# Kernel tuning notes

Measured on AMD Instinct MI355X. Metric: run time of the kernel, lower is better.

Reference implementation:

```python
import jax, jax.numpy as jnp
import numpy as np
from jax import lax

NUM_ENT = 100000
NUM_REL = 500
ENT_DIM = 100   # emb_dim1 * emb_dim2 = 10 * 10
REL_DIM = 2500  # 100 filters * 5 * 5
BATCH = 1024
EPS = 1e-5


def _bn(x, gamma, beta, axes):
    # training-mode batchnorm (batch statistics), matching torch BN in train mode
    mean = jnp.mean(x, axis=axes, keepdims=True)
    var = jnp.var(x, axis=axes, keepdims=True)
    shape = [1] * x.ndim
    ch_axis = [a for a in range(x.ndim) if a not in axes][0]
    shape[ch_axis] = x.shape[ch_axis]
    g = gamma.reshape(shape)
    b = beta.reshape(shape)
    return (x - mean) * g * lax.rsqrt(var + EPS) + b


def setup_inputs() -> dict:
    key = jax.random.key(0)
    ks = jax.random.split(key, 6)
    e1 = jax.random.randint(ks[0], (BATCH,), 0, NUM_ENT)
    rel = jax.random.randint(ks[1], (BATCH,), 0, NUM_REL)
    emb_e = jax.random.normal(ks[2], (NUM_ENT, ENT_DIM), jnp.float32) * 0.1
    emb_rel = jax.random.normal(ks[3], (NUM_REL, REL_DIM), jnp.float32) * 0.1
    fc_w = jax.random.normal(ks[4], (ENT_DIM, 100 * 6 * 6), jnp.float32) * 0.02
    fc_b = jnp.zeros((ENT_DIM,), jnp.float32)
    bias = jnp.zeros((NUM_ENT,), jnp.float32)
    return {
        "e1": e1, "rel": rel,
        "emb_e": emb_e, "emb_rel": emb_rel,
        "fc_w": fc_w, "fc_b": fc_b, "bias": bias,
        "g0": jnp.ones((1,), jnp.float32), "b0": jnp.zeros((1,), jnp.float32),
        "g1": jnp.ones((100,), jnp.float32), "b1": jnp.zeros((100,), jnp.float32),
        "grel": jnp.ones((REL_DIM,), jnp.float32), "brel": jnp.zeros((REL_DIM,), jnp.float32),
        "g2": jnp.ones((ENT_DIM,), jnp.float32), "b2": jnp.zeros((ENT_DIM,), jnp.float32),
    }


def reference(e1, rel, emb_e, emb_rel, fc_w, fc_b, bias, g0, b0, g1, b1, grel, brel, g2, b2):
    B = e1.shape[0]
    e = emb_e[e1].reshape(B, 1, 10, 10)          # [B,1,10,10]
    r = emb_rel[rel]                              # [B,2500]
    r = _bn(r, grel, brel, axes=(0,))
    e = _bn(e, g0, b0, axes=(0, 2, 3))
    # dropout layers are identity (inference)
    filters = r.reshape(B * 100, 1, 5, 5)         # per-sample dynamic filters
    # per-sample conv as a single grouped conv: groups = B
    x = lax.conv_general_dilated(
        e.reshape(1, B, 10, 10), filters,
        window_strides=(1, 1), padding='VALID',
        feature_group_count=B,
        dimension_numbers=('NCHW', 'OIHW', 'NCHW'))
    x = x.reshape(B, 100, 6, 6)
    x = jax.nn.relu(_bn(x, g1, b1, axes=(0, 2, 3)))
    x = x.reshape(B, -1) @ fc_w.T + fc_b          # [B,100]
    x = jax.nn.relu(_bn(x, g2, b2, axes=(0,)))
    logits = x @ emb_e.T + bias                   # [B,NUM_ENT] memory-bound
    return jax.nn.sigmoid(logits)
```

## Files before the change

kernel.cpp:

```cpp
#include <hip/hip_runtime.h>
#include <cstdint>

#define NENT 100000
#define EPS 1e-5f

constexpr long REL_A    = 0;
constexpr long REL_B    = 2500;
constexpr long EPART    = 5000;
constexpr long EAB      = 5040;
constexpr long A1O      = 5056;
constexpr long C1O      = 5156;
constexpr long PART_OFF = 5888;
constexpr long XBUF_OFF = 415488;
constexpr long XHAT_OFF = 4101888;
constexpr long PSTAT    = XBUF_OFF;

typedef __attribute__((ext_vector_type(8))) __bf16 bf16x8;
typedef __attribute__((ext_vector_type(4))) float  f32x4;

#define BARLK() asm volatile("s_waitcnt lgkmcnt(0)\n\ts_barrier" ::: "memory")

__device__ __forceinline__ unsigned short f2bf(float f) {
    unsigned int u = __float_as_uint(f);
    unsigned int r = (u + 0x7FFFu + ((u >> 16) & 1u)) >> 16;
    return (unsigned short)r;
}

__global__ void k_stats1(const int* __restrict__ rel, const float* __restrict__ emb_rel,
                         const int* __restrict__ e1, const float* __restrict__ emb_e,
                         float* __restrict__ ws) {
    __shared__ float shmem[512];
    int tid = threadIdx.x, blk = blockIdx.x;
    if (blk < 125) {
        int* cnti = (int*)shmem;
        for (int i = tid; i < 512; i += 256) cnti[i] = 0;
        __syncthreads();
        for (int i = tid; i < 1024; i += 256) atomicAdd(&cnti[rel[i]], 1);
        __syncthreads();
        float s[10], q[10];
#pragma unroll
        for (int k = 0; k < 10; k++) { s[k] = 0.f; q[k] = 0.f; }
#pragma unroll
        for (int rr = 0; rr < 4; rr++) {
            int r = blk * 4 + rr;
            float c = (float)cnti[r];
            if (c != 0.f) {
                const float* row = emb_rel + (long)r * 2500;
#pragma unroll
                for (int k = 0; k < 10; k++) {
                    int idx = tid + k * 256;
                    if (idx < 2500) {
                        float v = row[idx];
                        s[k] = fmaf(c, v, s[k]);
                        q[k] = fmaf(c * v, v, q[k]);
                    }
                }
            }
        }
        float* ps = ws + PSTAT + (long)blk * 5000;
#pragma unroll
        for (int k = 0; k < 10; k++) {
            int idx = tid + k * 256;
            if (idx < 2500) { ps[idx] = s[k]; ps[2500 + idx] = q[k]; }
        }
    } else if (blk < 141) {
        float* ps = shmem;
        __shared__ float pq[256];
        __shared__ int eidx[64];
        int bi = blk - 125;
        if (tid < 64) eidx[tid] = e1[bi * 64 + tid];
        __syncthreads();
        float s = 0.f, q = 0.f;
        for (int i = tid; i < 6400; i += 256) {
            int b = i / 100, d = i - b * 100;
            float v = emb_e[(long)eidx[b] * 100 + d];
            s += v; q += v * v;
        }
        ps[tid] = s; pq[tid] = q;
        __syncthreads();
        for (int off = 128; off > 0; off >>= 1) {
            if (tid < off) { ps[tid] += ps[tid + off]; pq[tid] += pq[tid + off]; }
            __syncthreads();
        }
        if (tid == 0) { ws[EPART + bi * 2] = ps[0]; ws[EPART + bi * 2 + 1] = pq[0]; }
    }
}

__global__ void k_stats2(const float* __restrict__ grel, const float* __restrict__ brel,
                         const float* __restrict__ g0, const float* __restrict__ b0,
                         float* __restrict__ ws) {
    __shared__ float ps[512], pq[512];
    int tid = threadIdx.x, blk = blockIdx.x;
    if (blk < 40) {
        int f = blk * 64 + (tid & 63);
        int g = tid >> 6;
        float s = 0.f, q = 0.f;
        for (int p = g; p < 125; p += 8) {
            s += ws[PSTAT + (long)p * 5000 + f];
            q += ws[PSTAT + (long)p * 5000 + 2500 + f];
        }
        ps[tid] = s; pq[tid] = q;
        __syncthreads();
        if (tid < 64) {
            float ss = 0.f, qq = 0.f;
#pragma unroll
            for (int k = 0; k < 8; k++) { ss += ps[tid + k * 64]; qq += pq[tid + k * 64]; }
            float mean = ss * (1.f / 1024.f);
            float var  = qq * (1.f / 1024.f) - mean * mean;
            float a = grel[f] * rsqrtf(var + EPS);
            ws[REL_A + f] = a;
            ws[REL_B + f] = brel[f] - mean * a;
        }
    } else if (tid == 0) {
        float s = 0.f, q = 0.f;
#pragma unroll
        for (int i = 0; i < 16; i++) { s += ws[EPART + 2 * i]; q += ws[EPART + 2 * i + 1]; }
        float mean = s * (1.f / 102400.f);
        float var  = q * (1.f / 102400.f) - mean * mean;
        float a = g0[0] * rsqrtf(var + EPS);
        ws[EAB]     = a;
        ws[EAB + 1] = b0[0] - mean * a;
    }
}

__global__ void k_conv(const int* __restrict__ e1, const int* __restrict__ rel,
                       const float* __restrict__ emb_e, const float* __restrict__ emb_rel,
                       const float* __restrict__ ws, float* __restrict__ xout,
                       float* __restrict__ bn1part) {
    __shared__ float es[100];
    __shared__ float flt[2500];
    __shared__ float prs[600], prq[600];
    int b = blockIdx.x, tid = threadIdx.x;
    float a0 = ws[EAB], c0 = ws[EAB + 1];
    long ebase = (long)e1[b] * 100;
    for (int i = tid; i < 100; i += 256) es[i] = a0 * emb_e[ebase + i] + c0;
    long rbase = (long)rel[b] * 2500;
    for (int i = tid; i < 2500; i += 256) flt[i] = ws[REL_A + i] * emb_rel[rbase + i] + ws[REL_B + i];
    __syncthreads();
    for (int u = tid; u < 600; u += 256) {
        int f = u / 6, oi = u - f * 6;
        float er[5][10];
#pragma unroll
        for (int p = 0; p < 5; p++)
#pragma unroll
            for (int c = 0; c < 10; c++) er[p][c] = es[(oi + p) * 10 + c];
        float fw[25];
#pragma unroll
        for (int k = 0; k < 25; k++) fw[k] = flt[f * 25 + k];
        float* dst = xout + (long)b * 3600 + f * 36 + oi * 6;
        float s6 = 0.f, q6 = 0.f;
#pragma unroll
        for (int oj = 0; oj < 6; oj++) {
            float acc = 0.f;
#pragma unroll
            for (int p = 0; p < 5; p++)
#pragma unroll
                for (int q = 0; q < 5; q++) acc += er[p][oj + q] * fw[p * 5 + q];
            dst[oj] = acc;
            s6 += acc; q6 = fmaf(acc, acc, q6);
        }
        prs[u] = s6; prq[u] = q6;
    }
    __syncthreads();
    if (tid < 100) {
        float s = 0.f, q = 0.f;
#pragma unroll
        for (int k = 0; k < 6; k++) { s += prs[tid * 6 + k]; q += prq[tid * 6 + k]; }
        bn1part[(long)tid * 1024 + b]         = s;
        bn1part[(long)(100 + tid) * 1024 + b] = q;
    }
}

__global__ void k_bn1r(const float* __restrict__ bn1part, const float* __restrict__ g1,
                       const float* __restrict__ b1, float* __restrict__ ws) {
    __shared__ float ps[256], pq[256];
    int f = blockIdx.x, tid = threadIdx.x;
    float s = 0.f, q = 0.f;
    for (int b = tid; b < 1024; b += 256) {
        s += bn1part[(long)f * 1024 + b];
        q += bn1part[(long)(100 + f) * 1024 + b];
    }
    ps[tid] = s; pq[tid] = q;
    __syncthreads();
    for (int off = 128; off > 0; off >>= 1) {
        if (tid < off) { ps[tid] += ps[tid + off]; pq[tid] += pq[tid + off]; }
        __syncthreads();
    }
    if (tid == 0) {
        float mean = ps[0] * (1.f / 36864.f);
        float var  = pq[0] * (1.f / 36864.f) - mean * mean;
        float a = g1[f] * rsqrtf(var + EPS);
        ws[A1O + f] = a;
        ws[C1O + f] = b1[f] - mean * a;
    }
}

__global__ void k_fc(const float* __restrict__ xbuf, const float* __restrict__ fc_w,
                     const float* __restrict__ ws, float* __restrict__ part) {
    __shared__ float a1s[100], c1s[100];
    __shared__ float xs[8][900];
    int tid = threadIdx.x;
    int sb = blockIdx.x, kc = blockIdx.y;
    if (tid < 100) { a1s[tid] = ws[A1O + tid]; c1s[tid] = ws[C1O + tid]; }
    __syncthreads();
    int b0s = sb * 8, k0 = kc * 900;
    for (int idx = tid; idx < 7200; idx += 256) {
        int s = idx / 900, k = idx - s * 900;
        int kg = k0 + k;
        int f = kg / 36;
        float v = xbuf[(long)(b0s + s) * 3600 + kg];
        v = a1s[f] * v + c1s[f];
        xs[s][k] = v > 0.f ? v : 0.f;
    }
    __syncthreads();
    int w = tid >> 6, l = tid & 63;
    int g = l >> 4, ks16 = l & 15;
    for (int t = 0; t < 7; t++) {
        int grp = w + 4 * t;
        if (grp >= 25) break;
        int j = grp * 4 + g;
        const float* wrow = fc_w + (long)j * 3600 + k0;
        float acc[8];
#pragma unroll
        for (int s = 0; s < 8; s++) acc[s] = 0.f;
#pragma unroll
        for (int i = 0; i < 15; i++) {
            int kk = ks16 + i * 16;
            if (kk < 225) {
                float4 w4 = *(const float4*)(wrow + kk * 4);
#pragma unroll
                for (int s = 0; s < 8; s++) {
                    float4 x4 = *(const float4*)(&xs[s][kk * 4]);
                    acc[s] += w4.x * x4.x + w4.y * x4.y + w4.z * x4.z + w4.w * x4.w;
                }
            }
        }
#pragma unroll
        for (int s = 0; s < 8; s++) {
            float v = acc[s];
            v += __shfl_xor(v, 1);
            v += __shfl_xor(v, 2);
            v += __shfl_xor(v, 4);
            v += __shfl_xor(v, 8);
            acc[s] = v;
        }
#pragma unroll
        for (int s = 0; s < 8; s++) {
            if (ks16 == s)
                part[((long)kc * 100 + j) * 1024 + b0s + s] = acc[s];
        }
    }
}

__global__ void k_bn2x(const float* __restrict__ part, const float* __restrict__ fc_b,
                       const float* __restrict__ g2, const float* __restrict__ b2,
                       unsigned short* __restrict__ xhat) {
    int j = blockIdx.x, tid = threadIdx.x;
    if (j >= 100) {
        for (int t = 0; t < 4; t++) xhat[(long)(tid + t * 256) * 128 + j] = 0;
        return;
    }
    __shared__ float ps[256], pq[256];
    __shared__ float ab[2];
    float v[4];
    float s = 0.f, q = 0.f;
#pragma unroll
    for (int t = 0; t < 4; t++) {
        int b = tid + t * 256;
        float x = part[(long)j * 1024 + b] + part[(long)(100 + j) * 1024 + b]
                + part[(long)(200 + j) * 1024 + b] + part[(long)(300 + j) * 1024 + b]
                + fc_b[j];
        v[t] = x; s += x; q += x * x;
    }
    ps[tid] = s; pq[tid] = q;
    __syncthreads();
    for (int off = 128; off > 0; off >>= 1) {
        if (tid < off) { ps[tid] += ps[tid + off]; pq[tid] += pq[tid + off]; }
        __syncthreads();
    }
    if (tid == 0) {
        float mean = ps[0] * (1.f / 1024.f);
        float var  = pq[0] * (1.f / 1024.f) - mean * mean;
        float a = g2[j] * rsqrtf(var + EPS);
        ab[0] = a; ab[1] = b2[j] - mean * a;
    }
    __syncthreads();
    float a = ab[0], c = ab[1];
#pragma unroll
    for (int t = 0; t < 4; t++) {
        float x = a * v[t] + c;
        x = x > 0.f ? x : 0.f;
        xhat[(long)(tid + t * 256) * 128 + j] = f2bf(x);
    }
}

__global__ void __launch_bounds__(256, 2)
k_gemm(const unsigned short* __restrict__ xhat, const float* __restrict__ emb_e,
       const float* __restrict__ bias, float* __restrict__ out) {
    __shared__ __align__(16) unsigned short Es[256 * 128];
    char* EsB = (char*)Es;
    int tid = threadIdx.x;
    int n0 = blockIdx.x * 256;

    {
        int r = tid;
        int g = n0 + r;
        unsigned int rowb = (unsigned)r * 256u;
        unsigned int sw = ((unsigned)r & 7u) << 4;
        ushort4 z; z.x = z.y = z.z = z.w = 0;
        if (g < NENT) {
            const float4* src = (const float4*)(emb_e + (long)g * 100);
#pragma unroll
            for (int i = 0; i < 25; i++) {
                float4 v = src[i];
                ushort4 h;
                h.x = f2bf(v.x); h.y = f2bf(v.y); h.z = f2bf(v.z); h.w = f2bf(v.w);
                *(ushort4*)(EsB + ((rowb + 8u * i) ^ sw)) = h;
            }
        } else {
#pragma unroll
            for (int i = 0; i < 25; i++) *(ushort4*)(EsB + ((rowb + 8u * i) ^ sw)) = z;
        }
#pragma unroll
        for (int zz = 0; zz < 7; zz++) *(ushort4*)(EsB + ((rowb + 200u + 8u * zz) ^ sw)) = z;
    }
    __syncthreads();

    int w = tid >> 6, l = tid & 63;
    int l15 = l & 15, l4 = l >> 4;

    bf16x8 Af[4][4];
#pragma unroll
    for (int fe = 0; fe < 4; fe++) {
        unsigned int r = (unsigned)(w * 64 + fe * 16 + l15);
        unsigned int base = r * 256u + (unsigned)(l4 * 16);
        unsigned int sw = (r & 7u) << 4;
#pragma unroll
        for (int ks = 0; ks < 4; ks++)
            Af[ks][fe] = *(const bf16x8*)(EsB + ((base + (unsigned)(ks * 64)) ^ sw));
    }
    BARLK();

    int colg = n0 + l * 4;
    bool colv = colg < NENT;
    f32x4 bb = colv ? *(const f32x4*)(bias + colg) : f32x4{0.f, 0.f, 0.f, 0.f};

    int xrow = l15 * 128 + l4 * 8;

    bf16x8 Bp[4];
#pragma unroll
    for (int fx = 0; fx < 4; fx++)
        Bp[fx] = *(const bf16x8*)(xhat + (long)(fx * 2048 + xrow));

    for (int chunk = 0; chunk < 16; ++chunk) {
        int m0 = chunk * 64;
        f32x4 acc[4][4];
#pragma unroll
        for (int fe = 0; fe < 4; fe++)
#pragma unroll
            for (int fx = 0; fx < 4; fx++) acc[fe][fx] = f32x4{0.f, 0.f, 0.f, 0.f};

#pragma unroll
        for (int fe = 0; fe < 4; fe++)
#pragma unroll
            for (int fx = 0; fx < 4; fx++)
                acc[fe][fx] = __builtin_amdgcn_mfma_f32_16x16x32_bf16(Af[0][fe], Bp[fx], acc[fe][fx], 0, 0, 0);

#pragma unroll
        for (int ks = 1; ks < 4; ++ks) {
            bf16x8 Bf[4];
#pragma unroll
            for (int fx = 0; fx < 4; fx++)
                Bf[fx] = *(const bf16x8*)(xhat + (long)(m0 * 128 + fx * 2048 + ks * 32 + xrow));
#pragma unroll
            for (int fe = 0; fe < 4; fe++)
#pragma unroll
                for (int fx = 0; fx < 4; fx++)
                    acc[fe][fx] = __builtin_amdgcn_mfma_f32_16x16x32_bf16(Af[ks][fe], Bf[fx], acc[fe][fx], 0, 0, 0);
        }

        if (chunk < 15) {
            int m0n = (chunk + 1) * 64;
#pragma unroll
            for (int fx = 0; fx < 4; fx++)
                Bp[fx] = *(const bf16x8*)(xhat + (long)(m0n * 128 + fx * 2048 + xrow));
        }

#pragma unroll
        for (int fe = 0; fe < 4; fe++) {
            unsigned int s = (unsigned)(w * 16 + fe * 4 + l4);
#pragma unroll
            for (int fx = 0; fx < 4; fx++) {
                unsigned int row = (unsigned)(fx * 16 + l15);
                *(f32x4*)(EsB + row * 1024u + ((s ^ (row & 7u)) * 16u)) = acc[fe][fx];
            }
        }
        BARLK();

#pragma unroll
        for (int pass = 0; pass < 16; pass++) {
            unsigned int row = (unsigned)(pass * 4 + w);
            f32x4 v = *(f32x4*)(EsB + row * 1024u + ((((unsigned)l) ^ (row & 7u)) * 16u));
            f32x4 o;
#pragma unroll
            for (int k = 0; k < 4; k++) {
                float x = v[k] + bb[k];
                float e = __builtin_amdgcn_exp2f(x * -1.44269504f);
                o[k] = __builtin_amdgcn_rcpf(1.0f + e);
            }
            if (colv)
                __builtin_nontemporal_store(o, (f32x4*)(out + (long)(m0 + row) * NENT + colg));
        }
        BARLK();
    }
}

extern "C" void kernel_launch(void* const* d_in, const int* in_sizes, int n_in,
                              void* d_out, int out_size, void* d_ws, size_t ws_size,
                              hipStream_t stream) {
    const int*   e1      = (const int*)d_in[0];
    const int*   rel     = (const int*)d_in[1];
    const float* emb_e   = (const float*)d_in[2];
    const float* emb_rel = (const float*)d_in[3];
    const float* fc_w    = (const float*)d_in[4];
    const float* fc_b    = (const float*)d_in[5];
    const float* bias    = (const float*)d_in[6];
    const float* g0      = (const float*)d_in[7];
    const float* b0      = (const float*)d_in[8];
    const float* g1      = (const float*)d_in[9];
    const float* b1      = (const float*)d_in[10];
    const float* grel    = (const float*)d_in[11];
    const float* brel    = (const float*)d_in[12];
    const float* g2      = (const float*)d_in[13];
    const float* b2      = (const float*)d_in[14];
    float* ws  = (float*)d_ws;
    float* out = (float*)d_out;

    hipLaunchKernelGGL(k_stats1, dim3(141), dim3(256), 0, stream, rel, emb_rel, e1, emb_e, ws);
    hipLaunchKernelGGL(k_stats2, dim3(41), dim3(512), 0, stream, grel, brel, g0, b0, ws);
    hipLaunchKernelGGL(k_conv, dim3(1024), dim3(256), 0, stream, e1, rel, emb_e, emb_rel,
                       ws, ws + XBUF_OFF, ws + PART_OFF);
    hipLaunchKernelGGL(k_bn1r, dim3(100), dim3(256), 0, stream, ws + PART_OFF, g1, b1, ws);
    hipLaunchKernelGGL(k_fc, dim3(128, 4), dim3(256), 0, stream, ws + XBUF_OFF, fc_w, ws, ws + PART_OFF);
    hipLaunchKernelGGL(k_bn2x, dim3(128), dim3(256), 0, stream, ws + PART_OFF, fc_b, g2, b2,
                       (unsigned short*)(ws + XHAT_OFF));
    hipLaunchKernelGGL(k_gemm, dim3(391), dim3(256), 0, stream,
                       (const unsigned short*)(ws + XHAT_OFF), emb_e, bias, out);
}
```

Measured before the change: 162.8 us.

## Split final GEMM over batch halves and halve LDS for higher occupancy

The logits GEMM grid is doubled so each block handles 256 entities but only half of the 1024 batch rows. Shared memory drops from 64KB to 32KB: the entity tile is staged in two 128-row phases, and the output transpose runs in two 32-row halves. Launch bounds now ask for 4 blocks per CU. This is meant to fill all CUs and hide the memory-bound output store latency with more resident waves. The cost is that each emb_e tile is loaded and converted twice, with extra barriers, and the register cap may cause spills.

```diff
diff --git a/kernel.cpp b/kernel.cpp
--- a/kernel.cpp
+++ b/kernel.cpp
@@ -294,66 +294,67 @@
     }
 }
 
-__global__ void __launch_bounds__(256, 2)
+__global__ void __launch_bounds__(256, 4)
 k_gemm(const unsigned short* __restrict__ xhat, const float* __restrict__ emb_e,
        const float* __restrict__ bias, float* __restrict__ out) {
-    __shared__ __align__(16) unsigned short Es[256 * 128];
+    __shared__ __align__(16) unsigned short Es[128 * 128];
     char* EsB = (char*)Es;
     int tid = threadIdx.x;
-    int n0 = blockIdx.x * 256;
-
-    {
-        int r = tid;
-        int g = n0 + r;
+    int nblk = blockIdx.x >> 1, mh = blockIdx.x & 1;
+    int n0 = nblk * 256;
+
+    int w = tid >> 6, l = tid & 63;
+    int l15 = l & 15, l4 = l >> 4;
+
+    bf16x8 Af[4][4];
+
+    for (int ph = 0; ph < 2; ph++) {
+        int r = tid >> 1, p = tid & 1;
+        int g = n0 + ph * 128 + r;
         unsigned int rowb = (unsigned)r * 256u;
         unsigned int sw = ((unsigned)r & 7u) << 4;
         ushort4 z; z.x = z.y = z.z = z.w = 0;
         if (g < NENT) {
             const float4* src = (const float4*)(emb_e + (long)g * 100);
-#pragma unroll
-            for (int i = 0; i < 25; i++) {
+            for (int i = p; i < 25; i += 2) {
                 float4 v = src[i];
                 ushort4 h;
                 h.x = f2bf(v.x); h.y = f2bf(v.y); h.z = f2bf(v.z); h.w = f2bf(v.w);
                 *(ushort4*)(EsB + ((rowb + 8u * i) ^ sw)) = h;
             }
         } else {
-#pragma unroll
-            for (int i = 0; i < 25; i++) *(ushort4*)(EsB + ((rowb + 8u * i) ^ sw)) = z;
-        }
-#pragma unroll
-        for (int zz = 0; zz < 7; zz++) *(ushort4*)(EsB + ((rowb + 200u + 8u * zz) ^ sw)) = z;
-    }
-    __syncthreads();
-
-    int w = tid >> 6, l = tid & 63;
-    int l15 = l & 15, l4 = l >> 4;
-
-    bf16x8 Af[4][4];
-#pragma unroll
-    for (int fe = 0; fe < 4; fe++) {
-        unsigned int r = (unsigned)(w * 64 + fe * 16 + l15);
-        unsigned int base = r * 256u + (unsigned)(l4 * 16);
-        unsigned int sw = (r & 7u) << 4;
-#pragma unroll
-        for (int ks = 0; ks < 4; ks++)
-            Af[ks][fe] = *(const bf16x8*)(EsB + ((base + (unsigned)(ks * 64)) ^ sw));
-    }
-    BARLK();
+            for (int i = p; i < 25; i += 2) *(ushort4*)(EsB + ((rowb + 8u * i) ^ sw)) = z;
+        }
+        for (int zz = p; zz < 7; zz += 2) *(ushort4*)(EsB + ((rowb + 200u + 8u * zz) ^ sw)) = z;
+        __syncthreads();
+        if ((w >> 1) == ph) {
+#pragma unroll
+            for (int fe = 0; fe < 4; fe++) {
+                unsigned int rr = (unsigned)((w & 1) * 64 + fe * 16 + l15);
+                unsigned int base = rr * 256u + (unsigned)(l4 * 16);
+                unsigned int sws = (rr & 7u) << 4;
+#pragma unroll
+                for (int ks = 0; ks < 4; ks++)
+                    Af[ks][fe] = *(const bf16x8*)(EsB + ((base + (unsigned)(ks * 64)) ^ sws));
+            }
+        }
+        __syncthreads();
+    }
 
     int colg = n0 + l * 4;
     bool colv = colg < NENT;
     f32x4 bb = colv ? *(const f32x4*)(bias + colg) : f32x4{0.f, 0.f, 0.f, 0.f};
 
     int xrow = l15 * 128 + l4 * 8;
+    long mbase = (long)mh * 512 * 128;
 
     bf16x8 Bp[4];
 #pragma unroll
     for (int fx = 0; fx < 4; fx++)
-        Bp[fx] = *(const bf16x8*)(xhat + (long)(fx * 2048 + xrow));
-
-    for (int chunk = 0; chunk < 16; ++chunk) {
-        int m0 = chunk * 64;
+        Bp[fx] = *(const bf16x8*)(xhat + mbase + (long)(fx * 2048 + xrow));
+
+    for (int chunk = 0; chunk < 8; ++chunk) {
+        int m0 = mh * 512 + chunk * 64;
         f32x4 acc[4][4];
 #pragma unroll
         for (int fe = 0; fe < 4; fe++)
@@ -371,7 +372,7 @@
             bf16x8 Bf[4];
 #pragma unroll
             for (int fx = 0; fx < 4; fx++)
-                Bf[fx] = *(const bf16x8*)(xhat + (long)(m0 * 128 + fx * 2048 + ks * 32 + xrow));
+                Bf[fx] = *(const bf16x8*)(xhat + mbase + (long)(chunk * 8192 + fx * 2048 + ks * 32 + xrow));
 #pragma unroll
             for (int fe = 0; fe < 4; fe++)
 #pragma unroll
@@ -379,39 +380,40 @@
                     acc[fe][fx] = __builtin_amdgcn_mfma_f32_16x16x32_bf16(Af[ks][fe], Bf[fx], acc[fe][fx], 0, 0, 0);
         }
 
-        if (chunk < 15) {
-            int m0n = (chunk + 1) * 64;
+        if (chunk < 7) {
 #pragma unroll
             for (int fx = 0; fx < 4; fx++)
-                Bp[fx] = *(const bf16x8*)(xhat + (long)(m0n * 128 + fx * 2048 + xrow));
-        }
-
-#pragma unroll
-        for (int fe = 0; fe < 4; fe++) {
-            unsigned int s = (unsigned)(w * 16 + fe * 4 + l4);
-#pragma unroll
-            for (int fx = 0; fx < 4; fx++) {
-                unsigned int row = (unsigned)(fx * 16 + l15);
-                *(f32x4*)(EsB + row * 1024u + ((s ^ (row & 7u)) * 16u)) = acc[fe][fx];
-            }
-        }
-        BARLK();
-
-#pragma unroll
-        for (int pass = 0; pass < 16; pass++) {
-            unsigned int row = (unsigned)(pass * 4 + w);
-            f32x4 v = *(f32x4*)(EsB + row * 1024u + ((((unsigned)l) ^ (row & 7u)) * 16u));
-            f32x4 o;
-#pragma unroll
-            for (int k = 0; k < 4; k++) {
-                float x = v[k] + bb[k];
-                float e = __builtin_amdgcn_exp2f(x * -1.44269504f);
-                o[k] = __builtin_amdgcn_rcpf(1.0f + e);
-            }
-            if (colv)
-                __builtin_nontemporal_store(o, (f32x4*)(out + (long)(m0 + row) * NENT + colg));
-        }
-        BARLK();
+                Bp[fx] = *(const bf16x8*)(xhat + mbase + (long)((chunk + 1) * 8192 + fx * 2048 + xrow));
+        }
+
+#pragma unroll
+        for (int h = 0; h < 2; h++) {
+#pragma unroll
+            for (int fe = 0; fe < 4; fe++) {
+                unsigned int s = (unsigned)(w * 16 + fe * 4 + l4);
+#pragma unroll
+                for (int fx2 = 0; fx2 < 2; fx2++) {
+                    unsigned int row = (unsigned)(fx2 * 16 + l15);
+                    *(f32x4*)(EsB + row * 1024u + ((s ^ (row & 7u)) * 16u)) = acc[fe][2 * h + fx2];
+                }
+            }
+            BARLK();
+#pragma unroll
+            for (int pass = 0; pass < 8; pass++) {
+                unsigned int row = (unsigned)(pass * 4 + w);
+                f32x4 v = *(f32x4*)(EsB + row * 1024u + ((((unsigned)l) ^ (row & 7u)) * 16u));
+                f32x4 o;
+#pragma unroll
+                for (int k = 0; k < 4; k++) {
+                    float x = v[k] + bb[k];
+                    float e = __builtin_amdgcn_exp2f(x * -1.44269504f);
+                    o[k] = __builtin_amdgcn_rcpf(1.0f + e);
+                }
+                if (colv)
+                    __builtin_nontemporal_store(o, (f32x4*)(out + (long)(m0 + h * 32 + row) * NENT + colg));
+            }
+            BARLK();
+        }
     }
 }
 
@@ -444,6 +446,6 @@
     hipLaunchKernelGGL(k_fc, dim3(128, 4), dim3(256), 0, stream, ws + XBUF_OFF, fc_w, ws, ws + PART_OFF);
     hipLaunchKernelGGL(k_bn2x, dim3(128), dim3(256), 0, stream, ws + PART_OFF, fc_b, g2, b2,
                        (unsigned short*)(ws + XHAT_OFF));
-    hipLaunchKernelGGL(k_gemm, dim3(391), dim3(256), 0, stream,
+    hipLaunchKernelGGL(k_gemm, dim3(782), dim3(256), 0, stream,
                        (const unsigned short*)(ws + XHAT_OFF), emb_e, bias, out);
 }
```

New measurement: 304.9 us. 1.87x slower.
